# Kernel tuning notes

Measured on AMD Instinct MI355X. Metric: run time of the kernel, lower is better.

Reference implementation:

```python
import jax, jax.numpy as jnp
import numpy as np

N_NODES = 10000
N_EDGES = 640000
IN_CH, HID, OUT_CH = 128, 128, 64


def _gcn_conv(x, edge_index, edge_weight, W, b, n_nodes):
    # PyG GCNConv (default add_self_loops=True, normalize=True, bias=True):
    #   A_hat = A + I ; D = rowsum(A_hat) ; norm_e = D^-1/2[src] * w_e * D^-1/2[dst]
    #   out[dst] += norm_e * (x @ W)[src] ; out += b
    src, dst = edge_index[0], edge_index[1]
    loop = jnp.arange(n_nodes, dtype=edge_index.dtype)
    src = jnp.concatenate([src, loop])
    dst = jnp.concatenate([dst, loop])
    w = jnp.concatenate([edge_weight, jnp.ones((n_nodes,), edge_weight.dtype)])
    deg = jax.ops.segment_sum(w, dst, num_segments=n_nodes)  # scatter on col
    dinv = jnp.where(deg > 0, jax.lax.rsqrt(deg), 0.0).astype(x.dtype)
    norm = dinv[src] * w * dinv[dst]  # [E+N]
    xw = x @ W  # dense GEMM [N, out]
    msg = norm[:, None] * xw[src]  # gather + scale [E+N, out]
    out = jax.ops.segment_sum(msg, dst, num_segments=n_nodes)  # scatter-add
    return out + b


def setup_inputs() -> dict:
    key = jax.random.key(0)
    ks = jax.random.split(key, 8)
    x = jax.random.normal(ks[0], (N_NODES, IN_CH), dtype=jnp.float32)
    edge_index = jax.random.randint(ks[1], (2, N_EDGES), 0, N_NODES, dtype=jnp.int64)
    edge_weight = jax.random.uniform(ks[2], (N_EDGES,), dtype=jnp.float32)
    W1 = jax.random.normal(ks[3], (IN_CH, HID), dtype=jnp.float32) * 0.05
    b1 = jnp.zeros((HID,), jnp.float32)
    W2 = jax.random.normal(ks[4], (HID, OUT_CH), dtype=jnp.float32) * 0.05
    b2 = jnp.zeros((OUT_CH,), jnp.float32)
    return {"x": x, "edge_index": edge_index, "edge_weight": edge_weight,
            "W1": W1, "b1": b1, "W2": W2, "b2": b2}


def reference(x, edge_index, edge_weight, W1, b1, W2, b2):
    h = _gcn_conv(x, edge_index, edge_weight, W1, b1, N_NODES)
    h = jax.nn.relu(h)
    out = _gcn_conv(h, edge_index, edge_weight, W2, b2, N_NODES)
    return out
```

## Files before the change

kernel.cpp:

```cpp
#include <hip/hip_runtime.h>
#include <math.h>

#define N_NODES 10000
#define N_EDGES 640000
#define ELLW    192

#define CHUNKS  128
#define CHUNK_E 5000
#define GB      625

typedef unsigned long long ull;
typedef unsigned int uint;
typedef unsigned short ushort;
typedef unsigned char uchar;

#define FIXED_SCALE 262144.0f


__device__ __forceinline__ float bf_lo(uint u) { return __uint_as_float(u << 16); }
__device__ __forceinline__ float bf_hi(uint u) { return __uint_as_float(u & 0xffff0000u); }
__device__ __forceinline__ ushort f2bf(float v) {
    uint u = __float_as_uint(v);
    uint r = u + 0x7fffu + ((u >> 16) & 1u);
    return (ushort)(r >> 16);
}

#define ACC8(n, r) \
    acc[0] = fmaf(n, bf_lo((r).x), acc[0]); acc[1] = fmaf(n, bf_hi((r).x), acc[1]); \
    acc[2] = fmaf(n, bf_lo((r).y), acc[2]); acc[3] = fmaf(n, bf_hi((r).y), acc[3]); \
    acc[4] = fmaf(n, bf_lo((r).z), acc[4]); acc[5] = fmaf(n, bf_hi((r).z), acc[5]); \
    acc[6] = fmaf(n, bf_lo((r).w), acc[6]); acc[7] = fmaf(n, bf_hi((r).w), acc[7]);

__global__ __launch_bounds__(256) void kernelA(const int* __restrict__ ei,
                                               const float* __restrict__ ew,
                                               uint* __restrict__ sd32,
                                               uint* __restrict__ blockcnt,
                                               const float* __restrict__ x,
                                               const float* __restrict__ W1,
                                               ushort* __restrict__ xw1b) {
    __shared__ __align__(16) uint smem[N_NODES];
    const int tid = threadIdx.x;
    if (blockIdx.x < CHUNKS) {
        const int c = blockIdx.x;
        __shared__ int sflag;
        if (tid == 0) sflag = 0;
        for (int i = tid; i < N_NODES; i += 256) smem[i] = 0u;
        __syncthreads();
        int a = (tid < 64) ? ei[2 * (c * CHUNK_E + tid) + 1] : 0;
        if (a) atomicOr(&sflag, 1);
        __syncthreads();
        const int f = sflag;
        const ull* ei64 = (const ull*)ei;
        for (int k = tid; k < CHUNK_E; k += 256) {
            int e = c * CHUNK_E + k;
            int s, d;
            if (f) { s = ei[e];        d = ei[N_EDGES + e]; }
            else   { s = (int)ei64[e]; d = (int)ei64[N_EDGES + e]; }
            float w = ew[e];
            uint fx = (uint)(w * FIXED_SCALE + 0.5f);
            uint old = atomicAdd(&smem[d], (1u << 24) | fx);
            uint r = (old >> 24) & 15u;
            sd32[e] = (r << 28) | ((uint)d << 14) | (uint)s;
        }
        __syncthreads();
        for (int i = tid; i < N_NODES; i += 256)
            blockcnt[c * N_NODES + i] = smem[i];
    } else {
        constexpr int K = 128, TM = 16, KT = 32, NCOL = 128, RPT = 8, LDA = KT + 4;
        float* sA = (float*)smem;
        float* sB = sA + TM * LDA;
        int blk = blockIdx.x - CHUNKS;
        int c = tid % NCOL, rr = tid / NCOL;
        int row0 = blk * TM;
        float acc[RPT];
#pragma unroll
        for (int r = 0; r < RPT; ++r) acc[r] = 0.0f;
        for (int k0 = 0; k0 < K; k0 += KT) {
            for (int i = tid; i < TM * KT; i += 256) {
                int r = i / KT, k = i % KT;
                int gr = row0 + r;
                sA[r * LDA + k] = (gr < N_NODES) ? x[gr * K + k0 + k] : 0.0f;
            }
            for (int i = tid; i < KT * NCOL; i += 256) {
                int k = i / NCOL, cc = i % NCOL;
                sB[k * NCOL + cc] = W1[(k0 + k) * NCOL + cc];
            }
            __syncthreads();
#pragma unroll
            for (int k = 0; k < KT; k += 4) {
                float b0 = sB[(k + 0) * NCOL + c];
                float b1 = sB[(k + 1) * NCOL + c];
                float b2 = sB[(k + 2) * NCOL + c];
                float b3 = sB[(k + 3) * NCOL + c];
#pragma unroll
                for (int r = 0; r < RPT; ++r) {
                    const float4 av = *(const float4*)&sA[(rr * RPT + r) * LDA + k];
                    acc[r] = fmaf(av.x, b0, acc[r]);
                    acc[r] = fmaf(av.y, b1, acc[r]);
                    acc[r] = fmaf(av.z, b2, acc[r]);
                    acc[r] = fmaf(av.w, b3, acc[r]);
                }
            }
            __syncthreads();
        }
#pragma unroll
        for (int r = 0; r < RPT; ++r) {
            int gr = row0 + rr * RPT + r;
            if (gr < N_NODES) xw1b[gr * NCOL + c] = f2bf(acc[r]);
        }
    }
}

__global__ __launch_bounds__(256) void scanB(const uint* __restrict__ blockcnt,
                                             uchar* __restrict__ base8,
                                             int* __restrict__ cnt_arr,
                                             float* __restrict__ dinv,
                                             const float* __restrict__ W2,
                                             uint* __restrict__ w2pg) {
    if (blockIdx.x >= 40) {
        int i = (blockIdx.x - 40) * 256 + threadIdx.x;
        int k2 = i >> 6, cc = i & 63;
        uint lo = (uint)f2bf(W2[(2 * k2) * 64 + cc]);
        uint hi = (uint)f2bf(W2[(2 * k2 + 1) * 64 + cc]);
        w2pg[i] = lo | (hi << 16);
        return;
    }
    int n = blockIdx.x * 256 + threadIdx.x;
    if (n >= N_NODES) return;
    uint wsum = 0;
    int run = 0;
#pragma unroll 8
    for (int c = 0; c < CHUNKS; ++c) {
        uint v = blockcnt[c * N_NODES + n];
        base8[c * N_NODES + n] = (uchar)run;
        run += (int)(v >> 24);
        wsum += v & 0xffffffu;
    }
    cnt_arr[n] = run;
    float dg = 1.0f + (float)wsum * (1.0f / FIXED_SCALE);
    dinv[n] = (float)(1.0 / sqrt((double)dg));
}

__global__ __launch_bounds__(256) void fillC(const uint* __restrict__ sd32,
                                             const float* __restrict__ ew,
                                             const uchar* __restrict__ base8,
                                             const float* __restrict__ dinv,
                                             ull* __restrict__ epack) {
    const int gid = blockIdx.x * 256 + threadIdx.x;
    const int stride = gridDim.x * 256;
    for (int e = gid; e < N_EDGES; e += stride) {
        uint sd = sd32[e];
        int s = (int)(sd & 0x3fffu);
        int d = (int)((sd >> 14) & 0x3fffu);
        int r = (int)(sd >> 28);
        int c = e / CHUNK_E;
        float nrm = dinv[s] * ew[e] * dinv[d];
        int slot = (int)base8[c * N_NODES + d] + r;
        if (slot < ELLW)
            epack[d * ELLW + slot] = ((ull)__float_as_uint(nrm) << 32) | (ull)(uint)s;
    }
}

__global__ __launch_bounds__(256, 6) void aggC(const ushort* __restrict__ xw1b,
                                               const ull* __restrict__ epack,
                                               const int* __restrict__ cnt_arr,
                                               const float* __restrict__ dinv,
                                               const float* __restrict__ b1,
                                               const uint* __restrict__ w2pg,
                                               ushort* __restrict__ xw2b) {
    __shared__ float hl[4][128];
    __shared__ uint w2p[64 * 64];
    const uint* __restrict__ xw32 = (const uint*)xw1b;
    const int tid = threadIdx.x;
    const int l = tid & 63;
    const int wv = tid >> 6;
    const int g = l >> 4;
    const int q = l & 15;
    const int node = blockIdx.x * 4 + wv;

    int cnt = __builtin_amdgcn_readfirstlane(cnt_arr[node]);
    if (cnt > ELLW) cnt = ELLW;
    const ull* ep = epack + (long)node * ELLW;

    ulonglong2 eA = *(const ulonglong2*)(ep + 2 * g);
    ulonglong2 eB = *(const ulonglong2*)(ep + 8 + 2 * g);

    for (int i = tid; i < 64 * 64; i += 256) w2p[i] = w2pg[i];

    float acc[8];
#pragma unroll
    for (int i = 0; i < 8; ++i) acc[i] = 0.0f;

    for (int j = 0; j < cnt; j += 16) {
        ulonglong2 nA = *(const ulonglong2*)(ep + j + 16 + 2 * g);
        ulonglong2 nB = *(const ulonglong2*)(ep + j + 24 + 2 * g);
        uint s0 = (uint)eA.x & 0x3fffu;
        uint s1 = (uint)eA.y & 0x3fffu;
        uint s2 = (uint)eB.x & 0x3fffu;
        uint s3 = (uint)eB.y & 0x3fffu;
        uint4 r0 = *(const uint4*)(xw32 + s0 * 64 + q * 4);
        uint4 r1 = *(const uint4*)(xw32 + s1 * 64 + q * 4);
        uint4 r2 = *(const uint4*)(xw32 + s2 * 64 + q * 4);
        uint4 r3 = *(const uint4*)(xw32 + s3 * 64 + q * 4);
        float n0 = (j + 2 * g     < cnt) ? __uint_as_float((uint)(eA.x >> 32)) : 0.0f;
        float n1 = (j + 2 * g + 1 < cnt) ? __uint_as_float((uint)(eA.y >> 32)) : 0.0f;
        float n2 = (j + 2 * g + 8 < cnt) ? __uint_as_float((uint)(eB.x >> 32)) : 0.0f;
        float n3 = (j + 2 * g + 9 < cnt) ? __uint_as_float((uint)(eB.y >> 32)) : 0.0f;
        ACC8(n0, r0)
        ACC8(n1, r1)
        ACC8(n2, r2)
        ACC8(n3, r3)
        eA = nA; eB = nB;
    }

#pragma unroll
    for (int i = 0; i < 8; ++i) {
        acc[i] += __shfl_xor(acc[i], 16, 64);
        acc[i] += __shfl_xor(acc[i], 32, 64);
    }

    float dn = dinv[node];
    float d2 = dn * dn;
    uint4 sv = *(const uint4*)(xw32 + node * 64 + q * 4);
    float4 b1a = *(const float4*)(b1 + 8 * q);
    float4 b1b = *(const float4*)(b1 + 8 * q + 4);
    if (g == 0) {
        hl[wv][8 * q + 0] = fmaxf(acc[0] + d2 * bf_lo(sv.x) + b1a.x, 0.0f);
        hl[wv][8 * q + 1] = fmaxf(acc[1] + d2 * bf_hi(sv.x) + b1a.y, 0.0f);
        hl[wv][8 * q + 2] = fmaxf(acc[2] + d2 * bf_lo(sv.y) + b1a.z, 0.0f);
        hl[wv][8 * q + 3] = fmaxf(acc[3] + d2 * bf_hi(sv.y) + b1a.w, 0.0f);
        hl[wv][8 * q + 4] = fmaxf(acc[4] + d2 * bf_lo(sv.z) + b1b.x, 0.0f);
        hl[wv][8 * q + 5] = fmaxf(acc[5] + d2 * bf_hi(sv.z) + b1b.y, 0.0f);
        hl[wv][8 * q + 6] = fmaxf(acc[6] + d2 * bf_lo(sv.w) + b1b.z, 0.0f);
        hl[wv][8 * q + 7] = fmaxf(acc[7] + d2 * bf_hi(sv.w) + b1b.w, 0.0f);
    }
    __syncthreads();

    float acc2 = 0.0f;
#pragma unroll 8
    for (int k2 = 0; k2 < 64; ++k2) {
        uint w = w2p[k2 * 64 + l];
        acc2 = fmaf(hl[wv][2 * k2],     bf_lo(w), acc2);
        acc2 = fmaf(hl[wv][2 * k2 + 1], bf_hi(w), acc2);
    }
    xw2b[node * 64 + l] = f2bf(acc2);
}

__global__ __launch_bounds__(256, 8) void agg2(const ushort* __restrict__ xw2b,
                                               const ull* __restrict__ epack,
                                               const int* __restrict__ cnt_arr,
                                               const float* __restrict__ dinv,
                                               const float* __restrict__ b2,
                                               float* __restrict__ out) {
    const uint* __restrict__ xw32 = (const uint*)xw2b;
    const int tid = threadIdx.x;
    const int l = tid & 63;
    const int wv = tid >> 6;
    const int g = l >> 3;
    const int q = l & 7;
    const int node = blockIdx.x * 4 + wv;

    int cnt = __builtin_amdgcn_readfirstlane(cnt_arr[node]);
    if (cnt > ELLW) cnt = ELLW;
    const ull* ep = epack + (long)node * ELLW;

    ulonglong2 eA = *(const ulonglong2*)(ep + 2 * g);

    float acc[8];
#pragma unroll
    for (int i = 0; i < 8; ++i) acc[i] = 0.0f;

    for (int j = 0; j < cnt; j += 16) {
        ulonglong2 nA = *(const ulonglong2*)(ep + j + 16 + 2 * g);
        uint s0 = (uint)eA.x & 0x3fffu;
        uint s1 = (uint)eA.y & 0x3fffu;
        uint4 r0 = *(const uint4*)(xw32 + s0 * 32 + q * 4);
        uint4 r1 = *(const uint4*)(xw32 + s1 * 32 + q * 4);
        float n0 = (j + 2 * g     < cnt) ? __uint_as_float((uint)(eA.x >> 32)) : 0.0f;
        float n1 = (j + 2 * g + 1 < cnt) ? __uint_as_float((uint)(eA.y >> 32)) : 0.0f;
        ACC8(n0, r0)
        ACC8(n1, r1)
        eA = nA;
    }

#pragma unroll
    for (int i = 0; i < 8; ++i) {
        acc[i] += __shfl_xor(acc[i], 8, 64);
        acc[i] += __shfl_xor(acc[i], 16, 64);
        acc[i] += __shfl_xor(acc[i], 32, 64);
    }

    float dn = dinv[node];
    float d2 = dn * dn;
    uint4 sv = *(const uint4*)(xw32 + node * 32 + q * 4);
    float4 b2a = *(const float4*)(b2 + 8 * q);
    float4 b2b = *(const float4*)(b2 + 8 * q + 4);
    if (g == 0) {
        float4 oa, ob;
        oa.x = acc[0] + d2 * bf_lo(sv.x) + b2a.x;
        oa.y = acc[1] + d2 * bf_hi(sv.x) + b2a.y;
        oa.z = acc[2] + d2 * bf_lo(sv.y) + b2a.z;
        oa.w = acc[3] + d2 * bf_hi(sv.y) + b2a.w;
        ob.x = acc[4] + d2 * bf_lo(sv.z) + b2b.x;
        ob.y = acc[5] + d2 * bf_hi(sv.z) + b2b.y;
        ob.z = acc[6] + d2 * bf_lo(sv.w) + b2b.z;
        ob.w = acc[7] + d2 * bf_hi(sv.w) + b2b.w;
        *(float4*)(out + node * 64 + 8 * q)     = oa;
        *(float4*)(out + node * 64 + 8 * q + 4) = ob;
    }
}

extern "C" void kernel_launch(void* const* d_in, const int* in_sizes, int n_in,
                              void* d_out, int out_size, void* d_ws, size_t ws_size,
                              hipStream_t stream) {
    const float* x  = (const float*)d_in[0];
    const int*   ei = (const int*)d_in[1];
    const float* ew = (const float*)d_in[2];
    const float* W1 = (const float*)d_in[3];
    const float* b1 = (const float*)d_in[4];
    const float* W2 = (const float*)d_in[5];
    const float* b2 = (const float*)d_in[6];
    float* out = (float*)d_out;

    char* ws = (char*)d_ws;
    ushort* xw1b    = (ushort*)(ws + 0);
    ushort* xw2b    = (ushort*)(ws + 5120000);
    ull*    epack   = (ull*)   (ws + 6400000);
    uint*   blockcnt= (uint*)  (ws + 21760000);
    uchar*  base8   = (uchar*) (ws + 26880000);
    uint*   sd32    = (uint*)  (ws + 28800000);
    int*    cnt_arr = (int*)   (ws + 31360000);
    float*  dinv    = (float*) (ws + 31400000);
    uint*   w2pg    = (uint*)  (ws + 31440000);

    kernelA<<<CHUNKS + GB, 256, 0, stream>>>(ei, ew, sd32, blockcnt, x, W1, xw1b);
    scanB<<<56, 256, 0, stream>>>(blockcnt, base8, cnt_arr, dinv, W2, w2pg);
    fillC<<<2500, 256, 0, stream>>>(sd32, ew, base8, dinv, epack);
    aggC<<<2500, 256, 0, stream>>>(xw1b, epack, cnt_arr, dinv, b1, w2pg, xw2b);
    agg2<<<2500, 256, 0, stream>>>(xw2b, epack, cnt_arr, dinv, b2, out);
}
```

Measured before the change: 139.4 us.

## Move GEMM into scan kernel, pack edge weight into sd64, use nontemporal epack access

The dense x@W1 GEMM moves out of the histogram kernel and into the scan kernel, so the histogram kernel runs only 128 blocks and the GEMM overlaps with the scan. The edge weight is packed with src/dst into a 64-bit record, so fillC no longer reads ew separately. fillC now handles one edge per thread and uses nontemporal loads and stores. aggC drops its per-block LDS copy of W2 and reads it from global memory, and both aggregation kernels use nontemporal loads for epack. The cost is a wider intermediate buffer and the risk that uncached W2 reads slow aggC's second GEMM.

```diff
diff --git a/kernel.cpp b/kernel.cpp
--- a/kernel.cpp
+++ b/kernel.cpp
@@ -13,6 +13,7 @@
 typedef unsigned int uint;
 typedef unsigned short ushort;
 typedef unsigned char uchar;
+typedef ull ull2v __attribute__((ext_vector_type(2)));
 
 #define FIXED_SCALE 262144.0f
 
@@ -24,6 +25,11 @@
     uint r = u + 0x7fffu + ((u >> 16) & 1u);
     return (ushort)(r >> 16);
 }
+__device__ __forceinline__ ulonglong2 ntld2(const ull* p) {
+    ull2v v = __builtin_nontemporal_load((const ull2v*)p);
+    ulonglong2 r; r.x = v.x; r.y = v.y;
+    return r;
+}
 
 #define ACC8(n, r) \
     acc[0] = fmaf(n, bf_lo((r).x), acc[0]); acc[1] = fmaf(n, bf_hi((r).x), acc[1]); \
@@ -31,45 +37,76 @@
     acc[4] = fmaf(n, bf_lo((r).z), acc[4]); acc[5] = fmaf(n, bf_hi((r).z), acc[5]); \
     acc[6] = fmaf(n, bf_lo((r).w), acc[6]); acc[7] = fmaf(n, bf_hi((r).w), acc[7]);
 
-__global__ __launch_bounds__(256) void kernelA(const int* __restrict__ ei,
-                                               const float* __restrict__ ew,
-                                               uint* __restrict__ sd32,
-                                               uint* __restrict__ blockcnt,
-                                               const float* __restrict__ x,
-                                               const float* __restrict__ W1,
-                                               ushort* __restrict__ xw1b) {
-    __shared__ __align__(16) uint smem[N_NODES];
+__global__ __launch_bounds__(256) void histK(const int* __restrict__ ei,
+                                             const float* __restrict__ ew,
+                                             ull* __restrict__ sd64,
+                                             uint* __restrict__ blockcnt) {
+    __shared__ uint smem[N_NODES];
+    __shared__ int sflag;
     const int tid = threadIdx.x;
-    if (blockIdx.x < CHUNKS) {
-        const int c = blockIdx.x;
-        __shared__ int sflag;
-        if (tid == 0) sflag = 0;
-        for (int i = tid; i < N_NODES; i += 256) smem[i] = 0u;
-        __syncthreads();
-        int a = (tid < 64) ? ei[2 * (c * CHUNK_E + tid) + 1] : 0;
-        if (a) atomicOr(&sflag, 1);
-        __syncthreads();
-        const int f = sflag;
-        const ull* ei64 = (const ull*)ei;
-        for (int k = tid; k < CHUNK_E; k += 256) {
-            int e = c * CHUNK_E + k;
-            int s, d;
-            if (f) { s = ei[e];        d = ei[N_EDGES + e]; }
-            else   { s = (int)ei64[e]; d = (int)ei64[N_EDGES + e]; }
-            float w = ew[e];
-            uint fx = (uint)(w * FIXED_SCALE + 0.5f);
-            uint old = atomicAdd(&smem[d], (1u << 24) | fx);
-            uint r = (old >> 24) & 15u;
-            sd32[e] = (r << 28) | ((uint)d << 14) | (uint)s;
+    const int c = blockIdx.x;
+    if (tid == 0) sflag = 0;
+    for (int i = tid; i < N_NODES; i += 256) smem[i] = 0u;
+    __syncthreads();
+    int a = (tid < 64) ? ei[2 * (c * CHUNK_E + tid) + 1] : 0;
+    if (a) atomicOr(&sflag, 1);
+    __syncthreads();
+    const int f = sflag;
+    const ull* ei64 = (const ull*)ei;
+    for (int k = tid; k < CHUNK_E; k += 256) {
+        int e = c * CHUNK_E + k;
+        int s, d;
+        if (f) { s = ei[e];        d = ei[N_EDGES + e]; }
+        else   { s = (int)ei64[e]; d = (int)ei64[N_EDGES + e]; }
+        float w = ew[e];
+        uint fx = (uint)(w * FIXED_SCALE + 0.5f);
+        uint old = atomicAdd(&smem[d], (1u << 24) | fx);
+        uint r = (old >> 24) & 15u;
+        sd64[e] = ((ull)__float_as_uint(w) << 32) |
+                  (ull)((r << 28) | ((uint)d << 14) | (uint)s);
+    }
+    __syncthreads();
+    for (int i = tid; i < N_NODES; i += 256)
+        blockcnt[c * N_NODES + i] = smem[i];
+}
+
+__global__ __launch_bounds__(256) void scangemm(const uint* __restrict__ blockcnt,
+                                                uchar* __restrict__ base8,
+                                                int* __restrict__ cnt_arr,
+                                                float* __restrict__ dinv,
+                                                const float* __restrict__ W2,
+                                                uint* __restrict__ w2pg,
+                                                const float* __restrict__ x,
+                                                const float* __restrict__ W1,
+                                                ushort* __restrict__ xw1b) {
+    __shared__ __align__(16) float smem[16 * 36 + 32 * 128];
+    const int tid = threadIdx.x;
+    if (blockIdx.x < 40) {
+        int n = blockIdx.x * 256 + tid;
+        if (n >= N_NODES) return;
+        uint wsum = 0;
+        int run = 0;
+#pragma unroll 8
+        for (int c = 0; c < CHUNKS; ++c) {
+            uint v = blockcnt[c * N_NODES + n];
+            base8[c * N_NODES + n] = (uchar)run;
+            run += (int)(v >> 24);
+            wsum += v & 0xffffffu;
         }
-        __syncthreads();
-        for (int i = tid; i < N_NODES; i += 256)
-            blockcnt[c * N_NODES + i] = smem[i];
+        cnt_arr[n] = run;
+        float dg = 1.0f + (float)wsum * (1.0f / FIXED_SCALE);
+        dinv[n] = (float)(1.0 / sqrt((double)dg));
+    } else if (blockIdx.x < 56) {
+        int i = (blockIdx.x - 40) * 256 + tid;
+        int k2 = i >> 6, cc = i & 63;
+        uint lo = (uint)f2bf(W2[(2 * k2) * 64 + cc]);
+        uint hi = (uint)f2bf(W2[(2 * k2 + 1) * 64 + cc]);
+        w2pg[i] = lo | (hi << 16);
     } else {
         constexpr int K = 128, TM = 16, KT = 32, NCOL = 128, RPT = 8, LDA = KT + 4;
-        float* sA = (float*)smem;
-        float* sB = sA + TM * LDA;
-        int blk = blockIdx.x - CHUNKS;
+        float* sA = smem;
+        float* sB = smem + TM * LDA;
+        int blk = blockIdx.x - 56;
         int c = tid % NCOL, rr = tid / NCOL;
         int row0 = blk * TM;
         float acc[RPT];
@@ -111,54 +148,24 @@
     }
 }
 
-__global__ __launch_bounds__(256) void scanB(const uint* __restrict__ blockcnt,
-                                             uchar* __restrict__ base8,
-                                             int* __restrict__ cnt_arr,
-                                             float* __restrict__ dinv,
-                                             const float* __restrict__ W2,
-                                             uint* __restrict__ w2pg) {
-    if (blockIdx.x >= 40) {
-        int i = (blockIdx.x - 40) * 256 + threadIdx.x;
-        int k2 = i >> 6, cc = i & 63;
-        uint lo = (uint)f2bf(W2[(2 * k2) * 64 + cc]);
-        uint hi = (uint)f2bf(W2[(2 * k2 + 1) * 64 + cc]);
-        w2pg[i] = lo | (hi << 16);
-        return;
-    }
-    int n = blockIdx.x * 256 + threadIdx.x;
-    if (n >= N_NODES) return;
-    uint wsum = 0;
-    int run = 0;
-#pragma unroll 8
-    for (int c = 0; c < CHUNKS; ++c) {
-        uint v = blockcnt[c * N_NODES + n];
-        base8[c * N_NODES + n] = (uchar)run;
-        run += (int)(v >> 24);
-        wsum += v & 0xffffffu;
-    }
-    cnt_arr[n] = run;
-    float dg = 1.0f + (float)wsum * (1.0f / FIXED_SCALE);
-    dinv[n] = (float)(1.0 / sqrt((double)dg));
-}
-
-__global__ __launch_bounds__(256) void fillC(const uint* __restrict__ sd32,
-                                             const float* __restrict__ ew,
+__global__ __launch_bounds__(256) void fillC(const ull* __restrict__ sd64,
                                              const uchar* __restrict__ base8,
                                              const float* __restrict__ dinv,
                                              ull* __restrict__ epack) {
-    const int gid = blockIdx.x * 256 + threadIdx.x;
-    const int stride = gridDim.x * 256;
-    for (int e = gid; e < N_EDGES; e += stride) {
-        uint sd = sd32[e];
-        int s = (int)(sd & 0x3fffu);
-        int d = (int)((sd >> 14) & 0x3fffu);
-        int r = (int)(sd >> 28);
-        int c = e / CHUNK_E;
-        float nrm = dinv[s] * ew[e] * dinv[d];
-        int slot = (int)base8[c * N_NODES + d] + r;
-        if (slot < ELLW)
-            epack[d * ELLW + slot] = ((ull)__float_as_uint(nrm) << 32) | (ull)(uint)s;
-    }
+    const int e = blockIdx.x * 256 + threadIdx.x;
+    if (e >= N_EDGES) return;
+    ull v = __builtin_nontemporal_load(&sd64[e]);
+    uint lo = (uint)v;
+    int s = (int)(lo & 0x3fffu);
+    int d = (int)((lo >> 14) & 0x3fffu);
+    int r = (int)(lo >> 28);
+    float w = __uint_as_float((uint)(v >> 32));
+    int c = e / CHUNK_E;
+    float nrm = dinv[s] * w * dinv[d];
+    int slot = (int)base8[c * N_NODES + d] + r;
+    if (slot < ELLW)
+        __builtin_nontemporal_store(((ull)__float_as_uint(nrm) << 32) | (ull)(uint)s,
+                                    &epack[(long)d * ELLW + slot]);
 }
 
 __global__ __launch_bounds__(256, 6) void aggC(const ushort* __restrict__ xw1b,
@@ -169,7 +176,6 @@
                                                const uint* __restrict__ w2pg,
                                                ushort* __restrict__ xw2b) {
     __shared__ float hl[4][128];
-    __shared__ uint w2p[64 * 64];
     const uint* __restrict__ xw32 = (const uint*)xw1b;
     const int tid = threadIdx.x;
     const int l = tid & 63;
@@ -182,18 +188,16 @@
     if (cnt > ELLW) cnt = ELLW;
     const ull* ep = epack + (long)node * ELLW;
 
-    ulonglong2 eA = *(const ulonglong2*)(ep + 2 * g);
-    ulonglong2 eB = *(const ulonglong2*)(ep + 8 + 2 * g);
-
-    for (int i = tid; i < 64 * 64; i += 256) w2p[i] = w2pg[i];
+    ulonglong2 eA = ntld2(ep + 2 * g);
+    ulonglong2 eB = ntld2(ep + 8 + 2 * g);
 
     float acc[8];
 #pragma unroll
     for (int i = 0; i < 8; ++i) acc[i] = 0.0f;
 
     for (int j = 0; j < cnt; j += 16) {
-        ulonglong2 nA = *(const ulonglong2*)(ep + j + 16 + 2 * g);
-        ulonglong2 nB = *(const ulonglong2*)(ep + j + 24 + 2 * g);
+        ulonglong2 nA = ntld2(ep + j + 16 + 2 * g);
+        ulonglong2 nB = ntld2(ep + j + 24 + 2 * g);
         uint s0 = (uint)eA.x & 0x3fffu;
         uint s1 = (uint)eA.y & 0x3fffu;
         uint s2 = (uint)eB.x & 0x3fffu;
@@ -239,7 +243,7 @@
     float acc2 = 0.0f;
 #pragma unroll 8
     for (int k2 = 0; k2 < 64; ++k2) {
-        uint w = w2p[k2 * 64 + l];
+        uint w = w2pg[k2 * 64 + l];
         acc2 = fmaf(hl[wv][2 * k2],     bf_lo(w), acc2);
         acc2 = fmaf(hl[wv][2 * k2 + 1], bf_hi(w), acc2);
     }
@@ -264,14 +268,14 @@
     if (cnt > ELLW) cnt = ELLW;
     const ull* ep = epack + (long)node * ELLW;
 
-    ulonglong2 eA = *(const ulonglong2*)(ep + 2 * g);
+    ulonglong2 eA = ntld2(ep + 2 * g);
 
     float acc[8];
 #pragma unroll
     for (int i = 0; i < 8; ++i) acc[i] = 0.0f;
 
     for (int j = 0; j < cnt; j += 16) {
-        ulonglong2 nA = *(const ulonglong2*)(ep + j + 16 + 2 * g);
+        ulonglong2 nA = ntld2(ep + j + 16 + 2 * g);
         uint s0 = (uint)eA.x & 0x3fffu;
         uint s1 = (uint)eA.y & 0x3fffu;
         uint4 r0 = *(const uint4*)(xw32 + s0 * 32 + q * 4);
@@ -328,14 +332,15 @@
     ull*    epack   = (ull*)   (ws + 6400000);
     uint*   blockcnt= (uint*)  (ws + 21760000);
     uchar*  base8   = (uchar*) (ws + 26880000);
-    uint*   sd32    = (uint*)  (ws + 28800000);
-    int*    cnt_arr = (int*)   (ws + 31360000);
-    float*  dinv    = (float*) (ws + 31400000);
-    uint*   w2pg    = (uint*)  (ws + 31440000);
-
-    kernelA<<<CHUNKS + GB, 256, 0, stream>>>(ei, ew, sd32, blockcnt, x, W1, xw1b);
-    scanB<<<56, 256, 0, stream>>>(blockcnt, base8, cnt_arr, dinv, W2, w2pg);
-    fillC<<<2500, 256, 0, stream>>>(sd32, ew, base8, dinv, epack);
+    ull*    sd64    = (ull*)   (ws + 28160000);
+    int*    cnt_arr = (int*)   (ws + 33280000);
+    float*  dinv    = (float*) (ws + 33320000);
+    uint*   w2pg    = (uint*)  (ws + 33360000);
+
+    histK<<<CHUNKS, 256, 0, stream>>>(ei, ew, sd64, blockcnt);
+    scangemm<<<56 + GB, 256, 0, stream>>>(blockcnt, base8, cnt_arr, dinv, W2, w2pg,
+                                          x, W1, xw1b);
+    fillC<<<2500, 256, 0, stream>>>(sd64, base8, dinv, epack);
     aggC<<<2500, 256, 0, stream>>>(xw1b, epack, cnt_arr, dinv, b1, w2pg, xw2b);
     agg2<<<2500, 256, 0, stream>>>(xw2b, epack, cnt_arr, dinv, b2, out);
 }
```

Measured after the change: 163.5 us. +17.3%, slower.
